# Kernel optimization log

Hardware: AMD Instinct MI355X
Metric: run time of the kernel (lower is better)

The kernel has to match this reference:

```python
import jax, jax.numpy as jnp
import numpy as np

N = 50000      # nodes
E = 800000     # edges
IN = 128       # in_channels
C = 32         # hidden_channels per head
H = 8          # heads
NC = 2         # num_classes
EPS = 1e-5     # batchnorm eps
SLOPE = 0.2    # leaky relu negative slope


def setup_inputs() -> dict:
    key = jax.random.key(0)
    ks = jax.random.split(key, 16)
    d = {}
    d["x"] = jax.random.normal(ks[0], (N, IN), dtype=jnp.float32)
    d["edge_index"] = jax.random.randint(ks[1], (2, E), 0, N, dtype=jnp.int64)
    # layer 0: IN -> H*C (concat)
    s0 = 1.0 / np.sqrt(IN)
    d["Wl0"] = jax.random.normal(ks[2], (IN, H * C), dtype=jnp.float32) * s0
    d["Wr0"] = jax.random.normal(ks[3], (IN, H * C), dtype=jnp.float32) * s0
    d["att0"] = jax.random.normal(ks[4], (H, C), dtype=jnp.float32) * (1.0 / np.sqrt(C))
    d["b0"] = jnp.zeros((H * C,), dtype=jnp.float32)
    d["g0"] = jnp.ones((H * C,), dtype=jnp.float32)
    d["be0"] = jnp.zeros((H * C,), dtype=jnp.float32)
    d["m0"] = jax.random.normal(ks[5], (H * C,), dtype=jnp.float32) * 0.1
    d["v0"] = jax.random.uniform(ks[6], (H * C,), dtype=jnp.float32, minval=0.5, maxval=1.5)
    # layer 1: H*C -> C (mean over heads, concat=False)
    s1 = 1.0 / np.sqrt(H * C)
    d["Wl1"] = jax.random.normal(ks[7], (H * C, H * C), dtype=jnp.float32) * s1
    d["Wr1"] = jax.random.normal(ks[8], (H * C, H * C), dtype=jnp.float32) * s1
    d["att1"] = jax.random.normal(ks[9], (H, C), dtype=jnp.float32) * (1.0 / np.sqrt(C))
    d["b1"] = jnp.zeros((C,), dtype=jnp.float32)
    d["g1"] = jnp.ones((C,), dtype=jnp.float32)
    d["be1"] = jnp.zeros((C,), dtype=jnp.float32)
    d["m1"] = jax.random.normal(ks[10], (C,), dtype=jnp.float32) * 0.1
    d["v1"] = jax.random.uniform(ks[11], (C,), dtype=jnp.float32, minval=0.5, maxval=1.5)
    # classifier C -> NC
    d["Wc"] = jax.random.normal(ks[12], (C, NC), dtype=jnp.float32) * (1.0 / np.sqrt(C))
    d["bc"] = jnp.zeros((NC,), dtype=jnp.float32)
    return d


def _gatv2_layer(x, src, dst, Wl, Wr, att, b, concat, num_nodes):
    # GATv2Conv (PyG semantics): x_l = source proj, x_r = target proj,
    # e_ij = att . LeakyReLU(x_l[j] + x_r[i]); softmax over incoming edges of i;
    # out_i = sum_j alpha_ij * x_l[j]. Self-loops are added (PyG default).
    nH, nC = att.shape
    xl = (x @ Wl).reshape(num_nodes, nH, nC)
    xr = (x @ Wr).reshape(num_nodes, nH, nC)
    e = xl[src] + xr[dst]                              # [E', H, C]
    e = jnp.where(e > 0, e, SLOPE * e)
    logits = jnp.einsum('ehc,hc->eh', e, att)          # [E', H]
    m = jax.ops.segment_max(logits, dst, num_segments=num_nodes)   # [N, H]
    ex = jnp.exp(logits - m[dst])
    denom = jax.ops.segment_sum(ex, dst, num_segments=num_nodes)   # [N, H]
    alpha = ex / denom[dst]                            # [E', H]
    msg = alpha[:, :, None] * xl[src]                  # [E', H, C]
    out = jax.ops.segment_sum(msg, dst, num_segments=num_nodes)    # [N, H, C]
    if concat:
        return out.reshape(num_nodes, nH * nC) + b
    return out.mean(axis=1) + b


def _bn(x, g, be, m, v):
    return (x - m) * jax.lax.rsqrt(v + EPS) * g + be


def reference(x, edge_index, Wl0, Wr0, att0, b0, g0, be0, m0, v0,
              Wl1, Wr1, att1, b1, g1, be1, m1, v1, Wc, bc):
    num_nodes = x.shape[0]
    loop = jnp.arange(num_nodes, dtype=edge_index.dtype)
    src = jnp.concatenate([edge_index[0], loop])
    dst = jnp.concatenate([edge_index[1], loop])
    h = _gatv2_layer(x, src, dst, Wl0, Wr0, att0, b0, True, num_nodes)
    h = _bn(h, g0, be0, m0, v0)
    h = jax.nn.elu(h)   # eval mode: dropout is identity
    h = _gatv2_layer(h, src, dst, Wl1, Wr1, att1, b1, False, num_nodes)
    h = _bn(h, g1, be1, m1, v1)
    return h @ Wc + bc
```

## Files before the change

### kernel.cpp

```cpp
#include <hip/hip_runtime.h>
#include <math.h>

#define N_NODES 50000
#define M_PAD   50048
#define E_EDGES 800000
#define IN_CH   128
#define C_CH    32
#define H_HEADS 8
#define HC      256
#define BN_EPS  1e-5f
#define SLOPE   0.2f

#define SCAN_CHUNK 512
#define SCAN_B     ((N_NODES + SCAN_CHUNK - 1) / SCAN_CHUNK)

typedef _Float16 f16x8 __attribute__((ext_vector_type(8)));
typedef _Float16 f16x4 __attribute__((ext_vector_type(4)));
typedef _Float16 f16x2 __attribute__((ext_vector_type(2)));
typedef float    f32x4 __attribute__((ext_vector_type(4)));


__global__ void k_init_deg(int* deg, int n) {
    int i = blockIdx.x * blockDim.x + threadIdx.x;
    if (i < n) deg[i] = 1;
}

__global__ void k_hist(const int* __restrict__ dst, int* deg, int e) {
    int i = blockIdx.x * blockDim.x + threadIdx.x;
    if (i < e) atomicAdd(&deg[dst[i]], 1);
}

__global__ __launch_bounds__(256) void k_scan_local(
        const int* __restrict__ deg, int* __restrict__ row_ptr,
        int* __restrict__ partials, int n) {
    __shared__ int sm[256];
    int t = threadIdx.x;
    int base = blockIdx.x * SCAN_CHUNK;
    int i0 = base + 2 * t, i1 = i0 + 1;
    int a = (i0 < n) ? deg[i0] : 0;
    int b = (i1 < n) ? deg[i1] : 0;
    int s = a + b;
    sm[t] = s;
    __syncthreads();
    #pragma unroll
    for (int off = 1; off < 256; off <<= 1) {
        int u = (t >= off) ? sm[t - off] : 0;
        __syncthreads();
        sm[t] += u;
        __syncthreads();
    }
    int excl = sm[t] - s;
    if (i0 < n) row_ptr[i0] = excl;
    if (i1 < n) row_ptr[i1] = excl + a;
    if (t == 255) partials[blockIdx.x] = sm[255];
}

__global__ __launch_bounds__(128) void k_scan_part(
        int* __restrict__ partials, int* __restrict__ row_ptr_n) {
    __shared__ int sm[128];
    int t = threadIdx.x;
    int v = (t < SCAN_B) ? partials[t] : 0;
    sm[t] = v;
    __syncthreads();
    #pragma unroll
    for (int off = 1; off < 128; off <<= 1) {
        int u = (t >= off) ? sm[t - off] : 0;
        __syncthreads();
        sm[t] += u;
        __syncthreads();
    }
    if (t < SCAN_B) partials[t] = sm[t] - v;
    if (t == 127) *row_ptr_n = sm[127];
}

__global__ void k_scan_add(int* __restrict__ row_ptr, int* __restrict__ cursor,
                           const int* __restrict__ partials, int n) {
    int i = blockIdx.x * blockDim.x + threadIdx.x;
    if (i < n) {
        int v = row_ptr[i] + partials[i / SCAN_CHUNK];
        row_ptr[i] = v;
        cursor[i] = v;
    }
}

__global__ void k_fill(const int* __restrict__ src, const int* __restrict__ dst,
                       int* cursor, int* csr_src, int e, int n) {
    int i = blockIdx.x * blockDim.x + threadIdx.x;
    if (i < e) {
        int d = dst[i];
        int p = atomicAdd(&cursor[d], 1);
        csr_src[p] = src[i];
    } else if (i < e + n) {
        int v = i - e;
        int p = atomicAdd(&cursor[v], 1);
        csr_src[p] = v;
    }
}


__global__ void k_split_w4(const float* __restrict__ Wl0, const float* __restrict__ Wr0,
                           const float* __restrict__ Wl1, const float* __restrict__ Wr1,
                           _Float16* __restrict__ W0lt, _Float16* __restrict__ W0rt,
                           _Float16* __restrict__ W1lt, _Float16* __restrict__ W1rt) {
    int t = blockIdx.x * blockDim.x + threadIdx.x;
    const float* W; _Float16* O; int K, rel;
    if (t < 32768)       { W = Wl0; O = W0lt; K = 128; rel = t; }
    else if (t < 65536)  { W = Wr0; O = W0rt; K = 128; rel = t - 32768; }
    else if (t < 131072) { W = Wl1; O = W1lt; K = 256; rel = t - 65536; }
    else if (t < 196608) { W = Wr1; O = W1rt; K = 256; rel = t - 131072; }
    else return;
    int n = rel / K, k = rel - n * K;
    O[rel] = (_Float16)W[(size_t)k * 256 + n];
}


#define BK  32
#define LDA 40

__device__ __forceinline__ f16x8 cvt_h8(float4 a, float4 b) {
    f16x8 v = { (_Float16)a.x, (_Float16)a.y, (_Float16)a.z, (_Float16)a.w,
                (_Float16)b.x, (_Float16)b.y, (_Float16)b.z, (_Float16)b.w };
    return v;
}

__global__ __launch_bounds__(256) void k_gemm_mfma(
        const _Float16* __restrict__ A16, const float* __restrict__ A32,
        const _Float16* __restrict__ W0t, const _Float16* __restrict__ W1t,
        _Float16* __restrict__ C0, _Float16* __restrict__ C1, int K) {
    const _Float16* Wt = blockIdx.z ? W1t : W0t;
    _Float16* C = blockIdx.z ? C1 : C0;
    __shared__ _Float16 As[128 * LDA];
    __shared__ _Float16 Bs[128 * LDA];
    int t = threadIdx.x;
    int lane = t & 63, wv = t >> 6;
    int quad = lane >> 4, r16 = lane & 15;
    size_t mBase = (size_t)blockIdx.x * 128;
    size_t nBase = (size_t)blockIdx.y * 128;
    int sr = t >> 2;
    int sc = (t & 3) * 8;
    f32x4 acc[2][8] = {};
    for (int k0 = 0; k0 < K; k0 += BK) {
        if (A32) {
            size_t r0 = mBase + sr, r1 = r0 + 64;
            float4 a0 = {0.f,0.f,0.f,0.f}, a1 = a0, b0 = a0, b1 = a0;
            if (r0 < N_NODES) {
                const float* g = A32 + r0 * K + k0 + sc;
                a0 = ((const float4*)g)[0];
                a1 = ((const float4*)g)[1];
            }
            if (r1 < N_NODES) {
                const float* g = A32 + r1 * K + k0 + sc;
                b0 = ((const float4*)g)[0];
                b1 = ((const float4*)g)[1];
            }
            *(f16x8*)&As[sr * LDA + sc]        = cvt_h8(a0, a1);
            *(f16x8*)&As[(sr + 64) * LDA + sc] = cvt_h8(b0, b1);
        } else {
            const _Float16* gA = A16 + (mBase + sr) * K + k0 + sc;
            *(f16x8*)&As[sr * LDA + sc]        = *(const f16x8*)gA;
            *(f16x8*)&As[(sr + 64) * LDA + sc] = *(const f16x8*)(gA + (size_t)64 * K);
        }
        const _Float16* gB = Wt + (nBase + sr) * K + k0 + sc;
        *(f16x8*)&Bs[sr * LDA + sc]        = *(const f16x8*)gB;
        *(f16x8*)&Bs[(sr + 64) * LDA + sc] = *(const f16x8*)(gB + (size_t)64 * K);
        __syncthreads();
        f16x8 av[2];
        #pragma unroll
        for (int mi = 0; mi < 2; ++mi) {
            int m = wv * 32 + mi * 16 + r16;
            av[mi] = *(f16x8*)&As[m * LDA + quad * 8];
        }
        #pragma unroll
        for (int ni = 0; ni < 8; ++ni) {
            int n = ni * 16 + r16;
            f16x8 bv = *(f16x8*)&Bs[n * LDA + quad * 8];
            #pragma unroll
            for (int mi = 0; mi < 2; ++mi)
                acc[mi][ni] = __builtin_amdgcn_mfma_f32_16x16x32_f16(av[mi], bv, acc[mi][ni], 0, 0, 0);
        }
        __syncthreads();
    }
    #pragma unroll
    for (int mi = 0; mi < 2; ++mi)
        #pragma unroll
        for (int r = 0; r < 4; ++r) {
            size_t row = mBase + wv * 32 + mi * 16 + quad * 4 + r;
            _Float16* cp = C + row * 256 + nBase + r16;
            #pragma unroll
            for (int ni = 0; ni < 8; ++ni)
                cp[ni * 16] = (_Float16)acc[mi][ni][r];
        }
}


__device__ __forceinline__ float edge_w16(f16x4 h, f16x4 xr, f16x4 att) {
    f16x4 e = h + xr;
    f16x4 es = e * (_Float16)SLOPE;
    f16x4 l = __builtin_elementwise_max(e, es);
#if __has_builtin(__builtin_amdgcn_fdot2)
    f16x2 l01 = __builtin_shufflevector(l, l, 0, 1);
    f16x2 l23 = __builtin_shufflevector(l, l, 2, 3);
    f16x2 a01 = __builtin_shufflevector(att, att, 0, 1);
    f16x2 a23 = __builtin_shufflevector(att, att, 2, 3);
    float p = __builtin_amdgcn_fdot2(l01, a01, 0.f, false);
    p = __builtin_amdgcn_fdot2(l23, a23, p, false);
#else
    float p = (float)l[0] * (float)att[0];
    p = fmaf((float)l[1], (float)att[1], p);
    p = fmaf((float)l[2], (float)att[2], p);
    p = fmaf((float)l[3], (float)att[3], p);
#endif
    p += __shfl_xor(p, 1);
    p += __shfl_xor(p, 2);
    p += __shfl_xor(p, 4);
    return __expf(p);
}

__device__ __forceinline__ float4 edge_accum(
        const f16x4* __restrict__ xl4, f16x4 xr_h, f16x4 att_h,
        const int* __restrict__ csr_src, int beg, int end, int lane) {
    const f16x4* xlp = xl4 + lane;
    float4 acc = {0.f, 0.f, 0.f, 0.f};
    float S = 0.f;
    int j = beg;
    for (; j + 4 <= end; j += 4) {
        int s0 = csr_src[j];
        int s1 = csr_src[j + 1];
        int s2 = csr_src[j + 2];
        int s3 = csr_src[j + 3];
        f16x4 h0 = xlp[(size_t)s0 * 64];
        f16x4 h1 = xlp[(size_t)s1 * 64];
        f16x4 h2 = xlp[(size_t)s2 * 64];
        f16x4 h3 = xlp[(size_t)s3 * 64];
        float w0 = edge_w16(h0, xr_h, att_h);
        float w1 = edge_w16(h1, xr_h, att_h);
        float w2 = edge_w16(h2, xr_h, att_h);
        float w3 = edge_w16(h3, xr_h, att_h);
        S += (w0 + w1) + (w2 + w3);
        acc.x = fmaf((float)h0[0], w0, acc.x); acc.y = fmaf((float)h0[1], w0, acc.y);
        acc.z = fmaf((float)h0[2], w0, acc.z); acc.w = fmaf((float)h0[3], w0, acc.w);
        acc.x = fmaf((float)h1[0], w1, acc.x); acc.y = fmaf((float)h1[1], w1, acc.y);
        acc.z = fmaf((float)h1[2], w1, acc.z); acc.w = fmaf((float)h1[3], w1, acc.w);
        acc.x = fmaf((float)h2[0], w2, acc.x); acc.y = fmaf((float)h2[1], w2, acc.y);
        acc.z = fmaf((float)h2[2], w2, acc.z); acc.w = fmaf((float)h2[3], w2, acc.w);
        acc.x = fmaf((float)h3[0], w3, acc.x); acc.y = fmaf((float)h3[1], w3, acc.y);
        acc.z = fmaf((float)h3[2], w3, acc.z); acc.w = fmaf((float)h3[3], w3, acc.w);
    }
    for (; j < end; ++j) {
        int s = csr_src[j];
        f16x4 hv = xlp[(size_t)s * 64];
        float w = edge_w16(hv, xr_h, att_h);
        S += w;
        acc.x = fmaf((float)hv[0], w, acc.x); acc.y = fmaf((float)hv[1], w, acc.y);
        acc.z = fmaf((float)hv[2], w, acc.z); acc.w = fmaf((float)hv[3], w, acc.w);
    }
    float inv = 1.f / S;
    acc.x *= inv; acc.y *= inv; acc.z *= inv; acc.w *= inv;
    return acc;
}

__device__ __forceinline__ f16x4 cvt_h4(float4 v) {
    f16x4 r = { (_Float16)v.x, (_Float16)v.y, (_Float16)v.z, (_Float16)v.w };
    return r;
}

__global__ __launch_bounds__(256) void k_edge0(
        const _Float16* __restrict__ xl, const _Float16* __restrict__ xr,
        const float* __restrict__ att,
        const int* __restrict__ row_ptr, const int* __restrict__ csr_src,
        const float* __restrict__ b0, const float* __restrict__ g0,
        const float* __restrict__ be0, const float* __restrict__ m0,
        const float* __restrict__ v0,
        _Float16* __restrict__ h0) {
    int lane = threadIdx.x & 63;
    int i = blockIdx.x * 4 + (threadIdx.x >> 6);
    const f16x4* xl4 = (const f16x4*)xl;
    f16x4 xr_h = ((const f16x4*)xr)[(size_t)i * 64 + lane];
    f16x4 att_h = cvt_h4(((const float4*)att)[lane]);
    int beg = row_ptr[i], end = row_ptr[i + 1];
    float4 r = edge_accum(xl4, xr_h, att_h, csr_src, beg, end, lane);
    float4 bb = ((const float4*)b0)[lane];
    float4 gg = ((const float4*)g0)[lane];
    float4 ee = ((const float4*)be0)[lane];
    float4 mm = ((const float4*)m0)[lane];
    float4 vv = ((const float4*)v0)[lane];
    float4 o;
    o.x = (r.x + bb.x - mm.x) * rsqrtf(vv.x + BN_EPS) * gg.x + ee.x;
    o.y = (r.y + bb.y - mm.y) * rsqrtf(vv.y + BN_EPS) * gg.y + ee.y;
    o.z = (r.z + bb.z - mm.z) * rsqrtf(vv.z + BN_EPS) * gg.z + ee.z;
    o.w = (r.w + bb.w - mm.w) * rsqrtf(vv.w + BN_EPS) * gg.w + ee.w;
    o.x = o.x > 0.f ? o.x : expm1f(o.x);
    o.y = o.y > 0.f ? o.y : expm1f(o.y);
    o.z = o.z > 0.f ? o.z : expm1f(o.z);
    o.w = o.w > 0.f ? o.w : expm1f(o.w);
    f16x4 hh = { (_Float16)o.x, (_Float16)o.y, (_Float16)o.z, (_Float16)o.w };
    ((f16x4*)h0)[(size_t)i * 64 + lane] = hh;
}

__global__ __launch_bounds__(256) void k_edge1(
        const _Float16* __restrict__ xl, const _Float16* __restrict__ xr,
        const float* __restrict__ att,
        const int* __restrict__ row_ptr, const int* __restrict__ csr_src,
        const float* __restrict__ b1, const float* __restrict__ g1,
        const float* __restrict__ be1, const float* __restrict__ m1,
        const float* __restrict__ v1,
        const float* __restrict__ Wc, const float* __restrict__ bc,
        float* __restrict__ out) {
    int lane = threadIdx.x & 63;
    int q = lane & 7;
    int i = blockIdx.x * 4 + (threadIdx.x >> 6);
    const f16x4* xl4 = (const f16x4*)xl;
    f16x4 xr_h = ((const f16x4*)xr)[(size_t)i * 64 + lane];
    f16x4 att_h = cvt_h4(((const float4*)att)[lane]);
    int beg = row_ptr[i], end = row_ptr[i + 1];
    float4 r = edge_accum(xl4, xr_h, att_h, csr_src, beg, end, lane);
    #pragma unroll
    for (int mask = 8; mask <= 32; mask <<= 1) {
        r.x += __shfl_xor(r.x, mask);
        r.y += __shfl_xor(r.y, mask);
        r.z += __shfl_xor(r.z, mask);
        r.w += __shfl_xor(r.w, mask);
    }
    float4 bb = ((const float4*)b1)[q];
    float4 gg = ((const float4*)g1)[q];
    float4 ee = ((const float4*)be1)[q];
    float4 mm = ((const float4*)m1)[q];
    float4 vv = ((const float4*)v1)[q];
    r.x = (r.x * 0.125f + bb.x - mm.x) * rsqrtf(vv.x + BN_EPS) * gg.x + ee.x;
    r.y = (r.y * 0.125f + bb.y - mm.y) * rsqrtf(vv.y + BN_EPS) * gg.y + ee.y;
    r.z = (r.z * 0.125f + bb.z - mm.z) * rsqrtf(vv.z + BN_EPS) * gg.z + ee.z;
    r.w = (r.w * 0.125f + bb.w - mm.w) * rsqrtf(vv.w + BN_EPS) * gg.w + ee.w;
    float4 wc0 = ((const float4*)Wc)[q * 2];
    float4 wc1 = ((const float4*)Wc)[q * 2 + 1];
    float o0 = r.x * wc0.x + r.y * wc0.z + r.z * wc1.x + r.w * wc1.z;
    float o1 = r.x * wc0.y + r.y * wc0.w + r.z * wc1.y + r.w * wc1.w;
    #pragma unroll
    for (int mask = 1; mask <= 4; mask <<= 1) {
        o0 += __shfl_xor(o0, mask);
        o1 += __shfl_xor(o1, mask);
    }
    if (lane == 0) {
        float2 ov = {o0 + bc[0], o1 + bc[1]};
        *(float2*)(out + (size_t)i * 2) = ov;
    }
}


extern "C" void kernel_launch(void* const* d_in, const int* in_sizes, int n_in,
                              void* d_out, int out_size, void* d_ws, size_t ws_size,
                              hipStream_t stream) {
    const float* x    = (const float*)d_in[0];
    const int*   ei   = (const int*)d_in[1];
    const float* Wl0  = (const float*)d_in[2];
    const float* Wr0  = (const float*)d_in[3];
    const float* att0 = (const float*)d_in[4];
    const float* b0   = (const float*)d_in[5];
    const float* g0   = (const float*)d_in[6];
    const float* be0  = (const float*)d_in[7];
    const float* m0   = (const float*)d_in[8];
    const float* v0   = (const float*)d_in[9];
    const float* Wl1  = (const float*)d_in[10];
    const float* Wr1  = (const float*)d_in[11];
    const float* att1 = (const float*)d_in[12];
    const float* b1   = (const float*)d_in[13];
    const float* g1   = (const float*)d_in[14];
    const float* be1  = (const float*)d_in[15];
    const float* m1   = (const float*)d_in[16];
    const float* v1   = (const float*)d_in[17];
    const float* Wc   = (const float*)d_in[18];
    const float* bc   = (const float*)d_in[19];
    float* out = (float*)d_out;

    const int N = N_NODES, E = E_EDGES;
    const int* srcp = ei;
    const int* dstp = ei + E;

    char* p = (char*)d_ws;
    _Float16* xlf = (_Float16*)p; p += (size_t)M_PAD * HC * 2;
    _Float16* xrf = (_Float16*)p; p += (size_t)M_PAD * HC * 2;
    _Float16* h0  = (_Float16*)p; p += (size_t)M_PAD * HC * 2;
    _Float16* W0lt = (_Float16*)p; p += (size_t)HC * IN_CH * 2;
    _Float16* W0rt = (_Float16*)p; p += (size_t)HC * IN_CH * 2;
    _Float16* W1lt = (_Float16*)p; p += (size_t)HC * HC * 2;
    _Float16* W1rt = (_Float16*)p; p += (size_t)HC * HC * 2;
    int* deg      = (int*)p;
    int* row_ptr  = deg + N;
    int* cursor   = row_ptr + (N + 1);
    int* partials = cursor + N;
    int* csr_src  = partials + ((SCAN_B + 3) & ~3);

    k_init_deg<<<(N + 255) / 256, 256, 0, stream>>>(deg, N);
    k_hist<<<(E + 255) / 256, 256, 0, stream>>>(dstp, deg, E);
    k_scan_local<<<SCAN_B, 256, 0, stream>>>(deg, row_ptr, partials, N);
    k_scan_part<<<1, 128, 0, stream>>>(partials, row_ptr + N);
    k_scan_add<<<(N + 255) / 256, 256, 0, stream>>>(row_ptr, cursor, partials, N);
    k_fill<<<(E + N + 255) / 256, 256, 0, stream>>>(srcp, dstp, cursor, csr_src, E, N);

    k_split_w4<<<768, 256, 0, stream>>>(Wl0, Wr0, Wl1, Wr1, W0lt, W0rt, W1lt, W1rt);

    dim3 ggrid(M_PAD / 128, 2, 2);
    k_gemm_mfma<<<ggrid, 256, 0, stream>>>(nullptr, x, W0lt, W0rt, xlf, xrf, IN_CH);
    k_edge0<<<N / 4, 256, 0, stream>>>(xlf, xrf, att0, row_ptr, csr_src,
                                       b0, g0, be0, m0, v0, h0);
    k_gemm_mfma<<<ggrid, 256, 0, stream>>>(h0, nullptr, W1lt, W1rt, xlf, xrf, HC);
    k_edge1<<<N / 4, 256, 0, stream>>>(xlf, xrf, att1, row_ptr, csr_src,
                                       b1, g1, be1, m1, v1, Wc, bc, out);
}
```

Before: 403.3 us.

## Fuse left/right projections per GEMM block and split edges across half-waves

The GEMM now computes both Wl and Wr projections in one 512-thread block, sharing the A tile load instead of launching separate z-blocks that each reload A. The edge kernels use 8-wide fp16 loads with each half-wave processing alternate edges, then combine the halves with a cross-lane shuffle. This doubles memory-level parallelism per node and folds log2(e) into the attention vector so exp2 can be used directly. BN scale/shift are precomputed per lane. Risks: higher register use in the GEMM, and extra shuffle overhead at the end of each node.

Measured after the change: 411.2 us. No clear change (+2.0%).

```diff
diff --git a/kernel.cpp b/kernel.cpp
--- a/kernel.cpp
+++ b/kernel.cpp
@@ -10,6 +10,7 @@
 #define HC      256
 #define BN_EPS  1e-5f
 #define SLOPE   0.2f
+#define LOG2E   1.44269504f
 
 #define SCAN_CHUNK 512
 #define SCAN_B     ((N_NODES + SCAN_CHUNK - 1) / SCAN_CHUNK)
@@ -18,6 +19,12 @@
 typedef _Float16 f16x4 __attribute__((ext_vector_type(4)));
 typedef _Float16 f16x2 __attribute__((ext_vector_type(2)));
 typedef float    f32x4 __attribute__((ext_vector_type(4)));
+
+#if __has_builtin(__builtin_amdgcn_exp2f)
+#define EXP2F(x) __builtin_amdgcn_exp2f(x)
+#else
+#define EXP2F(x) exp2f(x)
+#endif
 
 
 __global__ void k_init_deg(int* deg, int n) {
@@ -123,14 +130,13 @@
     return v;
 }
 
-__global__ __launch_bounds__(256) void k_gemm_mfma(
+__global__ __launch_bounds__(512) void k_gemm_mfma(
         const _Float16* __restrict__ A16, const float* __restrict__ A32,
         const _Float16* __restrict__ W0t, const _Float16* __restrict__ W1t,
         _Float16* __restrict__ C0, _Float16* __restrict__ C1, int K) {
-    const _Float16* Wt = blockIdx.z ? W1t : W0t;
-    _Float16* C = blockIdx.z ? C1 : C0;
-    __shared__ _Float16 As[128 * LDA];
-    __shared__ _Float16 Bs[128 * LDA];
+    __shared__ _Float16 As [128 * LDA];
+    __shared__ _Float16 Bs0[128 * LDA];
+    __shared__ _Float16 Bs1[128 * LDA];
     int t = threadIdx.x;
     int lane = t & 63, wv = t >> 6;
     int quad = lane >> 4, r16 = lane & 15;
@@ -138,129 +144,128 @@
     size_t nBase = (size_t)blockIdx.y * 128;
     int sr = t >> 2;
     int sc = (t & 3) * 8;
-    f32x4 acc[2][8] = {};
+    f32x4 acc0[8] = {}, acc1[8] = {};
     for (int k0 = 0; k0 < K; k0 += BK) {
         if (A32) {
-            size_t r0 = mBase + sr, r1 = r0 + 64;
-            float4 a0 = {0.f,0.f,0.f,0.f}, a1 = a0, b0 = a0, b1 = a0;
+            size_t r0 = mBase + sr;
+            float4 a0 = {0.f, 0.f, 0.f, 0.f}, a1 = a0;
             if (r0 < N_NODES) {
                 const float* g = A32 + r0 * K + k0 + sc;
                 a0 = ((const float4*)g)[0];
                 a1 = ((const float4*)g)[1];
             }
-            if (r1 < N_NODES) {
-                const float* g = A32 + r1 * K + k0 + sc;
-                b0 = ((const float4*)g)[0];
-                b1 = ((const float4*)g)[1];
-            }
-            *(f16x8*)&As[sr * LDA + sc]        = cvt_h8(a0, a1);
-            *(f16x8*)&As[(sr + 64) * LDA + sc] = cvt_h8(b0, b1);
+            *(f16x8*)&As[sr * LDA + sc] = cvt_h8(a0, a1);
         } else {
-            const _Float16* gA = A16 + (mBase + sr) * K + k0 + sc;
-            *(f16x8*)&As[sr * LDA + sc]        = *(const f16x8*)gA;
-            *(f16x8*)&As[(sr + 64) * LDA + sc] = *(const f16x8*)(gA + (size_t)64 * K);
-        }
-        const _Float16* gB = Wt + (nBase + sr) * K + k0 + sc;
-        *(f16x8*)&Bs[sr * LDA + sc]        = *(const f16x8*)gB;
-        *(f16x8*)&Bs[(sr + 64) * LDA + sc] = *(const f16x8*)(gB + (size_t)64 * K);
-        __syncthreads();
-        f16x8 av[2];
-        #pragma unroll
-        for (int mi = 0; mi < 2; ++mi) {
-            int m = wv * 32 + mi * 16 + r16;
-            av[mi] = *(f16x8*)&As[m * LDA + quad * 8];
-        }
+            *(f16x8*)&As[sr * LDA + sc] =
+                *(const f16x8*)(A16 + (size_t)(mBase + sr) * K + k0 + sc);
+        }
+        *(f16x8*)&Bs0[sr * LDA + sc] = *(const f16x8*)(W0t + (size_t)(nBase + sr) * K + k0 + sc);
+        *(f16x8*)&Bs1[sr * LDA + sc] = *(const f16x8*)(W1t + (size_t)(nBase + sr) * K + k0 + sc);
+        __syncthreads();
+        f16x8 av = *(f16x8*)&As[(wv * 16 + r16) * LDA + quad * 8];
         #pragma unroll
         for (int ni = 0; ni < 8; ++ni) {
-            int n = ni * 16 + r16;
-            f16x8 bv = *(f16x8*)&Bs[n * LDA + quad * 8];
-            #pragma unroll
-            for (int mi = 0; mi < 2; ++mi)
-                acc[mi][ni] = __builtin_amdgcn_mfma_f32_16x16x32_f16(av[mi], bv, acc[mi][ni], 0, 0, 0);
-        }
-        __syncthreads();
-    }
-    #pragma unroll
-    for (int mi = 0; mi < 2; ++mi)
+            f16x8 bv0 = *(f16x8*)&Bs0[(ni * 16 + r16) * LDA + quad * 8];
+            f16x8 bv1 = *(f16x8*)&Bs1[(ni * 16 + r16) * LDA + quad * 8];
+            acc0[ni] = __builtin_amdgcn_mfma_f32_16x16x32_f16(av, bv0, acc0[ni], 0, 0, 0);
+            acc1[ni] = __builtin_amdgcn_mfma_f32_16x16x32_f16(av, bv1, acc1[ni], 0, 0, 0);
+        }
+        __syncthreads();
+    }
+    #pragma unroll
+    for (int r = 0; r < 4; ++r) {
+        size_t row = mBase + wv * 16 + quad * 4 + r;
+        _Float16* cp0 = C0 + row * 256 + nBase + r16;
+        _Float16* cp1 = C1 + row * 256 + nBase + r16;
         #pragma unroll
-        for (int r = 0; r < 4; ++r) {
-            size_t row = mBase + wv * 32 + mi * 16 + quad * 4 + r;
-            _Float16* cp = C + row * 256 + nBase + r16;
-            #pragma unroll
-            for (int ni = 0; ni < 8; ++ni)
-                cp[ni * 16] = (_Float16)acc[mi][ni][r];
-        }
-}
-
-
-__device__ __forceinline__ float edge_w16(f16x4 h, f16x4 xr, f16x4 att) {
-    f16x4 e = h + xr;
-    f16x4 es = e * (_Float16)SLOPE;
-    f16x4 l = __builtin_elementwise_max(e, es);
+        for (int ni = 0; ni < 8; ++ni) {
+            cp0[ni * 16] = (_Float16)acc0[ni][r];
+            cp1[ni * 16] = (_Float16)acc1[ni][r];
+        }
+    }
+}
+
+
+__device__ __forceinline__ float edge_logit8(f16x8 h, f16x8 xr, f16x8 att) {
+    f16x8 e = h + xr;
+    f16x8 es = e * (_Float16)SLOPE;
+    f16x8 l = __builtin_elementwise_max(e, es);
 #if __has_builtin(__builtin_amdgcn_fdot2)
-    f16x2 l01 = __builtin_shufflevector(l, l, 0, 1);
-    f16x2 l23 = __builtin_shufflevector(l, l, 2, 3);
-    f16x2 a01 = __builtin_shufflevector(att, att, 0, 1);
-    f16x2 a23 = __builtin_shufflevector(att, att, 2, 3);
-    float p = __builtin_amdgcn_fdot2(l01, a01, 0.f, false);
-    p = __builtin_amdgcn_fdot2(l23, a23, p, false);
+    float p = __builtin_amdgcn_fdot2(__builtin_shufflevector(l, l, 0, 1),
+                                     __builtin_shufflevector(att, att, 0, 1), 0.f, false);
+    p = __builtin_amdgcn_fdot2(__builtin_shufflevector(l, l, 2, 3),
+                               __builtin_shufflevector(att, att, 2, 3), p, false);
+    p = __builtin_amdgcn_fdot2(__builtin_shufflevector(l, l, 4, 5),
+                               __builtin_shufflevector(att, att, 4, 5), p, false);
+    p = __builtin_amdgcn_fdot2(__builtin_shufflevector(l, l, 6, 7),
+                               __builtin_shufflevector(att, att, 6, 7), p, false);
 #else
-    float p = (float)l[0] * (float)att[0];
-    p = fmaf((float)l[1], (float)att[1], p);
-    p = fmaf((float)l[2], (float)att[2], p);
-    p = fmaf((float)l[3], (float)att[3], p);
+    float p = 0.f;
+    #pragma unroll
+    for (int j = 0; j < 8; ++j) p = fmaf((float)l[j], (float)att[j], p);
 #endif
     p += __shfl_xor(p, 1);
     p += __shfl_xor(p, 2);
-    p += __shfl_xor(p, 4);
-    return __expf(p);
-}
-
-__device__ __forceinline__ float4 edge_accum(
-        const f16x4* __restrict__ xl4, f16x4 xr_h, f16x4 att_h,
-        const int* __restrict__ csr_src, int beg, int end, int lane) {
-    const f16x4* xlp = xl4 + lane;
-    float4 acc = {0.f, 0.f, 0.f, 0.f};
+    return p;
+}
+
+__device__ __forceinline__ void edge_fma8(float* acc, f16x8 h, float w) {
+    #pragma unroll
+    for (int c = 0; c < 8; ++c) acc[c] = fmaf((float)h[c], w, acc[c]);
+}
+
+__device__ __forceinline__ float edge_accum8(
+        const f16x8* __restrict__ xl8q, f16x8 xr_h, f16x8 att_h,
+        const int* __restrict__ csr_src, int beg, int end, int half,
+        float* __restrict__ acc) {
     float S = 0.f;
     int j = beg;
     for (; j + 4 <= end; j += 4) {
-        int s0 = csr_src[j];
-        int s1 = csr_src[j + 1];
-        int s2 = csr_src[j + 2];
-        int s3 = csr_src[j + 3];
-        f16x4 h0 = xlp[(size_t)s0 * 64];
-        f16x4 h1 = xlp[(size_t)s1 * 64];
-        f16x4 h2 = xlp[(size_t)s2 * 64];
-        f16x4 h3 = xlp[(size_t)s3 * 64];
-        float w0 = edge_w16(h0, xr_h, att_h);
-        float w1 = edge_w16(h1, xr_h, att_h);
-        float w2 = edge_w16(h2, xr_h, att_h);
-        float w3 = edge_w16(h3, xr_h, att_h);
-        S += (w0 + w1) + (w2 + w3);
-        acc.x = fmaf((float)h0[0], w0, acc.x); acc.y = fmaf((float)h0[1], w0, acc.y);
-        acc.z = fmaf((float)h0[2], w0, acc.z); acc.w = fmaf((float)h0[3], w0, acc.w);
-        acc.x = fmaf((float)h1[0], w1, acc.x); acc.y = fmaf((float)h1[1], w1, acc.y);
-        acc.z = fmaf((float)h1[2], w1, acc.z); acc.w = fmaf((float)h1[3], w1, acc.w);
-        acc.x = fmaf((float)h2[0], w2, acc.x); acc.y = fmaf((float)h2[1], w2, acc.y);
-        acc.z = fmaf((float)h2[2], w2, acc.z); acc.w = fmaf((float)h2[3], w2, acc.w);
-        acc.x = fmaf((float)h3[0], w3, acc.x); acc.y = fmaf((float)h3[1], w3, acc.y);
-        acc.z = fmaf((float)h3[2], w3, acc.z); acc.w = fmaf((float)h3[3], w3, acc.w);
-    }
-    for (; j < end; ++j) {
-        int s = csr_src[j];
-        f16x4 hv = xlp[(size_t)s * 64];
-        float w = edge_w16(hv, xr_h, att_h);
-        S += w;
-        acc.x = fmaf((float)hv[0], w, acc.x); acc.y = fmaf((float)hv[1], w, acc.y);
-        acc.z = fmaf((float)hv[2], w, acc.z); acc.w = fmaf((float)hv[3], w, acc.w);
-    }
-    float inv = 1.f / S;
-    acc.x *= inv; acc.y *= inv; acc.z *= inv; acc.w *= inv;
-    return acc;
-}
-
-__device__ __forceinline__ f16x4 cvt_h4(float4 v) {
-    f16x4 r = { (_Float16)v.x, (_Float16)v.y, (_Float16)v.z, (_Float16)v.w };
+        int sa = csr_src[j],     sb = csr_src[j + 1];
+        int se = csr_src[j + 2], sd = csr_src[j + 3];
+        int s0 = half ? sb : sa;
+        int s1 = half ? sd : se;
+        f16x8 h0 = xl8q[(size_t)s0 * 32];
+        f16x8 h1 = xl8q[(size_t)s1 * 32];
+        float p0 = edge_logit8(h0, xr_h, att_h);
+        float p1 = edge_logit8(h1, xr_h, att_h);
+        float w0 = EXP2F(p0), w1 = EXP2F(p1);
+        S += w0 + w1;
+        edge_fma8(acc, h0, w0);
+        edge_fma8(acc, h1, w1);
+    }
+    int rem = end - j;
+    if (rem > 0) {
+        int sa = csr_src[j];
+        int sb = (rem > 1) ? csr_src[j + 1] : sa;
+        int s0 = half ? sb : sa;
+        f16x8 h0 = xl8q[(size_t)s0 * 32];
+        float p0 = edge_logit8(h0, xr_h, att_h);
+        float w0 = (half && rem < 2) ? 0.f : EXP2F(p0);
+        S += w0;
+        edge_fma8(acc, h0, w0);
+        if (rem == 3) {
+            int s1 = csr_src[j + 2];
+            f16x8 h1 = xl8q[(size_t)s1 * 32];
+            float p1 = edge_logit8(h1, xr_h, att_h);
+            float w1 = half ? 0.f : EXP2F(p1);
+            S += w1;
+            edge_fma8(acc, h1, w1);
+        }
+    }
+    #pragma unroll
+    for (int c = 0; c < 8; ++c) acc[c] += __shfl_xor(acc[c], 32);
+    S += __shfl_xor(S, 32);
+    return S;
+}
+
+__device__ __forceinline__ f16x8 att_load8(const float* __restrict__ att, int q) {
+    f32x4 a0 = ((const f32x4*)att)[q * 2];
+    f32x4 a1 = ((const f32x4*)att)[q * 2 + 1];
+    f16x8 r = { (_Float16)(a0[0] * LOG2E), (_Float16)(a0[1] * LOG2E),
+                (_Float16)(a0[2] * LOG2E), (_Float16)(a0[3] * LOG2E),
+                (_Float16)(a1[0] * LOG2E), (_Float16)(a1[1] * LOG2E),
+                (_Float16)(a1[2] * LOG2E), (_Float16)(a1[3] * LOG2E) };
     return r;
 }
 
@@ -273,28 +278,39 @@
         const float* __restrict__ v0,
         _Float16* __restrict__ h0) {
     int lane = threadIdx.x & 63;
-    int i = blockIdx.x * 4 + (threadIdx.x >> 6);
-    const f16x4* xl4 = (const f16x4*)xl;
-    f16x4 xr_h = ((const f16x4*)xr)[(size_t)i * 64 + lane];
-    f16x4 att_h = cvt_h4(((const float4*)att)[lane]);
+    int q = lane & 31, half = lane >> 5;
+    int i = __builtin_amdgcn_readfirstlane(blockIdx.x * 4 + (threadIdx.x >> 6));
+    const f16x8* xl8q = (const f16x8*)xl + q;
+    f16x8 xr_h = ((const f16x8*)xr)[(size_t)i * 32 + q];
+    f16x8 att_h = att_load8(att, q);
+    float scv[8], shv[8];
+    #pragma unroll
+    for (int k = 0; k < 2; ++k) {
+        f32x4 bb = ((const f32x4*)b0)[q * 2 + k];
+        f32x4 gg = ((const f32x4*)g0)[q * 2 + k];
+        f32x4 ee = ((const f32x4*)be0)[q * 2 + k];
+        f32x4 mm = ((const f32x4*)m0)[q * 2 + k];
+        f32x4 vv = ((const f32x4*)v0)[q * 2 + k];
+        #pragma unroll
+        for (int jj = 0; jj < 4; ++jj) {
+            float s = rsqrtf(vv[jj] + BN_EPS) * gg[jj];
+            scv[k * 4 + jj] = s;
+            shv[k * 4 + jj] = (bb[jj] - mm[jj]) * s + ee[jj];
+        }
+    }
     int beg = row_ptr[i], end = row_ptr[i + 1];
-    float4 r = edge_accum(xl4, xr_h, att_h, csr_src, beg, end, lane);
-    float4 bb = ((const float4*)b0)[lane];
-    float4 gg = ((const float4*)g0)[lane];
-    float4 ee = ((const float4*)be0)[lane];
-    float4 mm = ((const float4*)m0)[lane];
-    float4 vv = ((const float4*)v0)[lane];
-    float4 o;
-    o.x = (r.x + bb.x - mm.x) * rsqrtf(vv.x + BN_EPS) * gg.x + ee.x;
-    o.y = (r.y + bb.y - mm.y) * rsqrtf(vv.y + BN_EPS) * gg.y + ee.y;
-    o.z = (r.z + bb.z - mm.z) * rsqrtf(vv.z + BN_EPS) * gg.z + ee.z;
-    o.w = (r.w + bb.w - mm.w) * rsqrtf(vv.w + BN_EPS) * gg.w + ee.w;
-    o.x = o.x > 0.f ? o.x : expm1f(o.x);
-    o.y = o.y > 0.f ? o.y : expm1f(o.y);
-    o.z = o.z > 0.f ? o.z : expm1f(o.z);
-    o.w = o.w > 0.f ? o.w : expm1f(o.w);
-    f16x4 hh = { (_Float16)o.x, (_Float16)o.y, (_Float16)o.z, (_Float16)o.w };
-    ((f16x4*)h0)[(size_t)i * 64 + lane] = hh;
+    float acc[8] = {};
+    float S = edge_accum8(xl8q, xr_h, att_h, csr_src, beg, end, half, acc);
+    float inv = 1.f / S;
+    f16x8 hh;
+    #pragma unroll
+    for (int c = 0; c < 8; ++c) {
+        float o = acc[c] * inv * scv[c] + shv[c];
+        o = o > 0.f ? o : expm1f(o);
+        hh[c] = (_Float16)o;
+    }
+    if (half == 0)
+        ((f16x8*)h0)[(size_t)i * 32 + q] = hh;
 }
 
 __global__ __launch_bounds__(256) void k_edge1(
@@ -307,38 +323,43 @@
         const float* __restrict__ Wc, const float* __restrict__ bc,
         float* __restrict__ out) {
     int lane = threadIdx.x & 63;
-    int q = lane & 7;
-    int i = blockIdx.x * 4 + (threadIdx.x >> 6);
-    const f16x4* xl4 = (const f16x4*)xl;
-    f16x4 xr_h = ((const f16x4*)xr)[(size_t)i * 64 + lane];
-    f16x4 att_h = cvt_h4(((const float4*)att)[lane]);
+    int q = lane & 31, half = lane >> 5, cb = q & 3;
+    int i = __builtin_amdgcn_readfirstlane(blockIdx.x * 4 + (threadIdx.x >> 6));
+    const f16x8* xl8q = (const f16x8*)xl + q;
+    f16x8 xr_h = ((const f16x8*)xr)[(size_t)i * 32 + q];
+    f16x8 att_h = att_load8(att, q);
     int beg = row_ptr[i], end = row_ptr[i + 1];
-    float4 r = edge_accum(xl4, xr_h, att_h, csr_src, beg, end, lane);
-    #pragma unroll
-    for (int mask = 8; mask <= 32; mask <<= 1) {
-        r.x += __shfl_xor(r.x, mask);
-        r.y += __shfl_xor(r.y, mask);
-        r.z += __shfl_xor(r.z, mask);
-        r.w += __shfl_xor(r.w, mask);
-    }
-    float4 bb = ((const float4*)b1)[q];
-    float4 gg = ((const float4*)g1)[q];
-    float4 ee = ((const float4*)be1)[q];
-    float4 mm = ((const float4*)m1)[q];
-    float4 vv = ((const float4*)v1)[q];
-    r.x = (r.x * 0.125f + bb.x - mm.x) * rsqrtf(vv.x + BN_EPS) * gg.x + ee.x;
-    r.y = (r.y * 0.125f + bb.y - mm.y) * rsqrtf(vv.y + BN_EPS) * gg.y + ee.y;
-    r.z = (r.z * 0.125f + bb.z - mm.z) * rsqrtf(vv.z + BN_EPS) * gg.z + ee.z;
-    r.w = (r.w * 0.125f + bb.w - mm.w) * rsqrtf(vv.w + BN_EPS) * gg.w + ee.w;
-    float4 wc0 = ((const float4*)Wc)[q * 2];
-    float4 wc1 = ((const float4*)Wc)[q * 2 + 1];
-    float o0 = r.x * wc0.x + r.y * wc0.z + r.z * wc1.x + r.w * wc1.z;
-    float o1 = r.x * wc0.y + r.y * wc0.w + r.z * wc1.y + r.w * wc1.w;
-    #pragma unroll
-    for (int mask = 1; mask <= 4; mask <<= 1) {
-        o0 += __shfl_xor(o0, mask);
-        o1 += __shfl_xor(o1, mask);
-    }
+    float acc[8] = {};
+    float S = edge_accum8(xl8q, xr_h, att_h, csr_src, beg, end, half, acc);
+    float inv = 1.f / S;
+    float r[8];
+    #pragma unroll
+    for (int c = 0; c < 8; ++c) r[c] = acc[c] * inv;
+    #pragma unroll
+    for (int mask = 4; mask <= 16; mask <<= 1)
+        #pragma unroll
+        for (int c = 0; c < 8; ++c) r[c] += __shfl_xor(r[c], mask);
+    float o0 = 0.f, o1 = 0.f;
+    #pragma unroll
+    for (int k = 0; k < 2; ++k) {
+        f32x4 bb = ((const f32x4*)b1)[cb * 2 + k];
+        f32x4 gg = ((const f32x4*)g1)[cb * 2 + k];
+        f32x4 ee = ((const f32x4*)be1)[cb * 2 + k];
+        f32x4 mm = ((const f32x4*)m1)[cb * 2 + k];
+        f32x4 vv = ((const f32x4*)v1)[cb * 2 + k];
+        #pragma unroll
+        for (int jj = 0; jj < 4; ++jj) {
+            int c = k * 4 + jj;
+            float s = rsqrtf(vv[jj] + BN_EPS) * gg[jj];
+            float o = r[c] * (0.125f * s) + (bb[jj] - mm[jj]) * s + ee[jj];
+            int ch = cb * 8 + c;
+            float2 w = ((const float2*)Wc)[ch];
+            o0 = fmaf(o, w.x, o0);
+            o1 = fmaf(o, w.y, o1);
+        }
+    }
+    o0 += __shfl_xor(o0, 1); o0 += __shfl_xor(o0, 2);
+    o1 += __shfl_xor(o1, 1); o1 += __shfl_xor(o1, 2);
     if (lane == 0) {
         float2 ov = {o0 + bc[0], o1 + bc[1]};
         *(float2*)(out + (size_t)i * 2) = ov;
@@ -398,11 +419,11 @@
 
     k_split_w4<<<768, 256, 0, stream>>>(Wl0, Wr0, Wl1, Wr1, W0lt, W0rt, W1lt, W1rt);
 
-    dim3 ggrid(M_PAD / 128, 2, 2);
-    k_gemm_mfma<<<ggrid, 256, 0, stream>>>(nullptr, x, W0lt, W0rt, xlf, xrf, IN_CH);
+    dim3 ggrid(M_PAD / 128, 2);
+    k_gemm_mfma<<<ggrid, 512, 0, stream>>>(nullptr, x, W0lt, W0rt, xlf, xrf, IN_CH);
     k_edge0<<<N / 4, 256, 0, stream>>>(xlf, xrf, att0, row_ptr, csr_src,
                                        b0, g0, be0, m0, v0, h0);
-    k_gemm_mfma<<<ggrid, 256, 0, stream>>>(h0, nullptr, W1lt, W1rt, xlf, xrf, HC);
+    k_gemm_mfma<<<ggrid, 512, 0, stream>>>(h0, nullptr, W1lt, W1rt, xlf, xrf, HC);
     k_edge1<<<N / 4, 256, 0, stream>>>(xlf, xrf, att1, row_ptr, csr_src,
                                        b1, g1, be1, m1, v1, Wc, bc, out);
 }
```
